# Performance work log

Measured on AMD Instinct MI355X. Metric: run time of the kernel, lower is better.

Reference implementation:

```python
import jax, jax.numpy as jnp
import numpy as np

B, S, D = 2, 2048, 1024
H = 16
HD = D // H  # 64


def setup_inputs() -> dict:
    key = jax.random.key(0)
    ks = jax.random.split(key, 9)
    scale = 1.0 / np.sqrt(D)
    x = jax.random.normal(ks[0], (B, S, D), dtype=jnp.float32)
    Wq = jax.random.normal(ks[1], (D, D), dtype=jnp.float32) * scale
    bq = jnp.zeros((D,), dtype=jnp.float32)
    Wk = jax.random.normal(ks[2], (D, D), dtype=jnp.float32) * scale
    bk = jnp.zeros((D,), dtype=jnp.float32)
    Wv = jax.random.normal(ks[3], (D, D), dtype=jnp.float32) * scale
    bv = jnp.zeros((D,), dtype=jnp.float32)
    Wo = jax.random.normal(ks[4], (D, D), dtype=jnp.float32) * scale
    bo = jnp.zeros((D,), dtype=jnp.float32)
    return {"x": x, "Wq": Wq, "bq": bq, "Wk": Wk, "bk": bk,
            "Wv": Wv, "bv": bv, "Wo": Wo, "bo": bo}


def reference(x, Wq, bq, Wk, bk, Wv, bv, Wo, bo):
    b, s, d = x.shape
    # QKV projections (PhotonicCore == dim->dim linear)
    Q = x @ Wq + bq
    K = x @ Wk + bk
    V = x @ Wv + bv
    # [B, H, S, HD]
    Q = Q.reshape(b, s, H, HD).transpose(0, 2, 1, 3)
    K = K.reshape(b, s, H, HD).transpose(0, 2, 1, 3)
    V = V.reshape(b, s, H, HD).transpose(0, 2, 1, 3)
    # full [B, H, S, S] scores, exactly as the original (unfused) module
    scores = jnp.einsum("bhqd,bhkd->bhqk", Q, K) / jnp.sqrt(jnp.asarray(HD, x.dtype))
    weights = jax.nn.softmax(scores, axis=-1)
    attn = jnp.einsum("bhqk,bhkd->bhqd", weights, V)
    attn = attn.transpose(0, 2, 1, 3).reshape(b, s, d)
    return attn @ Wo + bo
```

## Files before the change

### kernel.cpp

```cpp
#include <hip/hip_runtime.h>
#include <stdint.h>

typedef unsigned short u16;
typedef unsigned int u32;
typedef unsigned long long u64;
typedef __bf16 bf16x8 __attribute__((ext_vector_type(8)));
typedef float f32x4 __attribute__((ext_vector_type(4)));
typedef unsigned short u16x8 __attribute__((ext_vector_type(8)));
typedef unsigned short u16x4 __attribute__((ext_vector_type(4)));

#define QSCALE 0.1803368801111204f

static __device__ __forceinline__ u16 f2bf(float f) {
  unsigned u = __builtin_bit_cast(unsigned, f);
  u += 0x7fffu + ((u >> 16) & 1u);
  return (u16)(u >> 16);
}

static __device__ __forceinline__ bf16x8 ldfrag(const u16* p) {
  return *reinterpret_cast<const bf16x8*>(p);
}

static __device__ __forceinline__ void gll16(const u16* g, u16* l) {
  __builtin_amdgcn_global_load_lds(
      (const __attribute__((address_space(1))) void*)g,
      (__attribute__((address_space(3))) void*)l, 16, 0, 0);
}

static __device__ __forceinline__ u32 cvt_pk_bf16(float lo, float hi) {
  u32 r;
  asm("v_cvt_pk_bf16_f32 %0, %1, %2" : "=v"(r) : "v"(lo), "v"(hi));
  return r;
}

static __device__ __forceinline__ float fexp2(float x) {
  return __builtin_amdgcn_exp2f(x);
}

static __device__ __forceinline__ float fm3(float a, float b, float c) {
  return fmaxf(fmaxf(a, b), c);
}

__global__ __launch_bounds__(256) void cast_x_kernel(const float* __restrict__ x,
                                                     u16* __restrict__ xb) {
  int i = (blockIdx.x * 256 + threadIdx.x) * 8;
  const float4* p = reinterpret_cast<const float4*>(x + i);
  float4 a = p[0], b = p[1];
  u16x8 o;
  o[0] = f2bf(a.x); o[1] = f2bf(a.y); o[2] = f2bf(a.z); o[3] = f2bf(a.w);
  o[4] = f2bf(b.x); o[5] = f2bf(b.y); o[6] = f2bf(b.z); o[7] = f2bf(b.w);
  *reinterpret_cast<u16x8*>(xb + i) = o;
}

__global__ __launch_bounds__(256) void transpose_w_kernel(
    const float* __restrict__ Wq, const float* __restrict__ Wk,
    const float* __restrict__ Wv, const float* __restrict__ Wo,
    u16* __restrict__ WT) {
  __shared__ float tile[64][65];
  int z = blockIdx.z;
  const float* W = (z == 0) ? Wq : (z == 1) ? Wk : (z == 2) ? Wv : Wo;
  float wscale = (z == 0) ? QSCALE : 1.0f;
  u16* out = WT + (size_t)z * 1024 * 1024;
  int k0 = blockIdx.y * 64, n0 = blockIdx.x * 64;
  int t = threadIdx.x;
  int rr = t >> 4;
  int cc = (t & 15) * 4;
#pragma unroll
  for (int j = 0; j < 4; ++j) {
    int r = rr + 16 * j;
    float4 v = *reinterpret_cast<const float4*>(W + (size_t)(k0 + r) * 1024 + n0 + cc);
    tile[r][cc + 0] = v.x; tile[r][cc + 1] = v.y;
    tile[r][cc + 2] = v.z; tile[r][cc + 3] = v.w;
  }
  __syncthreads();
#pragma unroll
  for (int j = 0; j < 4; ++j) {
    int nl = rr + 16 * j;
    u16x4 o;
#pragma unroll
    for (int i2 = 0; i2 < 4; ++i2) o[i2] = f2bf(tile[cc + i2][nl] * wscale);
    *reinterpret_cast<u16x4*>(out + (size_t)(n0 + nl) * 1024 + k0 + cc) = o;
  }
}

template <int MODE>
static __device__ __forceinline__ void qkv_body(
    u16* smem, const u16* __restrict__ A, const u16* __restrict__ Wt,
    const float* __restrict__ bias, float bscale, u16* __restrict__ Out) {
  int t = threadIdx.x;
  int lane = t & 63, wave = t >> 6;
  int g = lane >> 4, c = lane & 15;
  int m0 = blockIdx.y * 128, n0 = blockIdx.x * 128;
  int wm = (wave >> 1) * 32, wn = (wave & 1) * 64;

  f32x4 acc[2][4] = {};

  const u16* Ag = A + (size_t)(m0 + (t >> 2)) * 1024 + (t & 3) * 8;
  const u16* Bg = Wt + (size_t)(n0 + (t >> 2)) * 1024 + (t & 3) * 8;

  u16* dstA = smem + t * 8;
  u16* dstB = smem + 4096 + t * 8;
  const int afo = (wm + c) * 32 + g * 8;
  const int bfo = 4096 + (wn + c) * 32 + g * 8;

  gll16(Ag, dstA);
  gll16(Bg, dstB);
  gll16(Ag + 32, dstA + 8192);
  gll16(Bg + 32, dstB + 8192);
  asm volatile("s_waitcnt vmcnt(2)" ::: "memory");
  __builtin_amdgcn_s_barrier();
  asm volatile("" ::: "memory");

  int cur = 0;
  for (int st = 0; st < 32; ++st) {
    if (st <= 29) {
      int nb = cur + 2; if (nb >= 3) nb -= 3;
      gll16(Ag + (st + 2) * 32, dstA + nb * 8192);
      gll16(Bg + (st + 2) * 32, dstB + nb * 8192);
    }
    const u16* buf = smem + cur * 8192;
    bf16x8 af[2], bfr[4];
#pragma unroll
    for (int i = 0; i < 2; ++i) af[i] = ldfrag(buf + afo + 16 * i * 32);
#pragma unroll
    for (int j = 0; j < 4; ++j) bfr[j] = ldfrag(buf + bfo + 16 * j * 32);
    __builtin_amdgcn_s_setprio(1);
#pragma unroll
    for (int i = 0; i < 2; ++i)
#pragma unroll
      for (int j = 0; j < 4; ++j) {
        if (MODE == 2)
          acc[i][j] = __builtin_amdgcn_mfma_f32_16x16x32_bf16(af[i], bfr[j], acc[i][j], 0, 0, 0);
        else
          acc[i][j] = __builtin_amdgcn_mfma_f32_16x16x32_bf16(bfr[j], af[i], acc[i][j], 0, 0, 0);
      }
    __builtin_amdgcn_s_setprio(0);

    if (st <= 29)
      asm volatile("s_waitcnt vmcnt(2)" ::: "memory");
    else if (st == 30)
      asm volatile("s_waitcnt vmcnt(0)" ::: "memory");
    if (st < 31) {
      __builtin_amdgcn_s_barrier();
      asm volatile("" ::: "memory");
    }
    ++cur; if (cur == 3) cur = 0;
  }

  if (MODE == 0) {
    int nj[4], hj[4], dj[4];
    f32x4 bbj[4];
#pragma unroll
    for (int j = 0; j < 4; ++j) {
      nj[j] = n0 + wn + 16 * j + 4 * g;
      hj[j] = nj[j] >> 6; dj[j] = nj[j] & 63;
      f32x4 bb = *reinterpret_cast<const f32x4*>(&bias[nj[j]]);
#pragma unroll
      for (int r = 0; r < 4; ++r) bbj[j][r] = bb[r] * bscale;
    }
#pragma unroll
    for (int i = 0; i < 2; ++i) {
      int m = m0 + wm + 16 * i + c;
      int b2 = m >> 11, s2 = m & 2047;
#pragma unroll
      for (int j = 0; j < 4; ++j) {
        u16x4 o4;
#pragma unroll
        for (int r = 0; r < 4; ++r) o4[r] = f2bf(acc[i][j][r] + bbj[j][r]);
        *reinterpret_cast<u16x4*>(
            Out + ((size_t)(b2 * 16 + hj[j]) * 2048 + s2) * 64 + dj[j]) = o4;
      }
    }
  } else {
    float bvj[4];
#pragma unroll
    for (int j = 0; j < 4; ++j) bvj[j] = bias[n0 + wn + 16 * j + c];
    u16* tb = smem;
    int b2 = m0 >> 11, s0 = m0 & 2047;
    int rdrow = t >> 3;
    int slot = t & 7;
    int sh_base = ((wave >> 1) & 1) * 32;
    __syncthreads();
#pragma unroll
    for (int half = 0; half < 2; ++half) {
      if ((wave >> 2) == half) {
#pragma unroll
        for (int i = 0; i < 2; ++i)
#pragma unroll
          for (int j = 0; j < 4; ++j) {
            u16x4 o4;
#pragma unroll
            for (int r = 0; r < 4; ++r) o4[r] = f2bf(acc[i][j][r] + bvj[j]);
            *reinterpret_cast<u16x4*>(
                &tb[(wn + 16 * j + c) * 72 + sh_base + 16 * i + 4 * g]) = o4;
          }
      }
      __syncthreads();
#pragma unroll
      for (int k = 0; k < 2; ++k) {
        int row = rdrow + 64 * k;
        u16x8 v = *reinterpret_cast<const u16x8*>(&tb[row * 72 + slot * 8]);
        int n = n0 + row, h2 = n >> 6, d2 = n & 63;
        *reinterpret_cast<u16x8*>(
            Out + ((size_t)(b2 * 16 + h2) * 64 + d2) * 2048 + s0 + half * 64 + slot * 8) = v;
      }
      if (half == 0) __syncthreads();
    }
  }
}

__global__ __launch_bounds__(512) void qkv_gemm_kernel(
    const u16* __restrict__ xb, const u16* __restrict__ WT,
    const float* __restrict__ bq, const float* __restrict__ bk,
    const float* __restrict__ bv,
    u16* __restrict__ Q, u16* __restrict__ K, u16* __restrict__ V) {
  __shared__ u16 smem[24576];
  int z = blockIdx.z;
  if (z == 0)      qkv_body<0>(smem, xb, WT, bq, QSCALE, Q);
  else if (z == 1) qkv_body<0>(smem, xb, WT + (size_t)1024 * 1024, bk, 1.0f, K);
  else             qkv_body<2>(smem, xb, WT + (size_t)2 * 1024 * 1024, bv, 1.0f, V);
}

__global__ __launch_bounds__(512) void oproj_kernel(
    const u16* __restrict__ A, const u16* __restrict__ Wt,
    const float* __restrict__ bias, float* __restrict__ out) {
  __shared__ u16 smem[24576];
  int t = threadIdx.x;
  int lane = t & 63, wave = t >> 6;
  int g = lane >> 4, c = lane & 15;
  int m0 = blockIdx.y * 128, n0 = blockIdx.x * 128;
  int wm = (wave >> 1) * 32, wn = (wave & 1) * 64;

  f32x4 acc[2][4] = {};

  const u16* Ag = A + (size_t)(m0 + (t >> 2)) * 1024 + (t & 3) * 8;
  const u16* Bg = Wt + (size_t)(n0 + (t >> 2)) * 1024 + (t & 3) * 8;
  u16* dstA = smem + t * 8;
  u16* dstB = smem + 4096 + t * 8;
  const int afo = (wm + c) * 32 + g * 8;
  const int bfo = 4096 + (wn + c) * 32 + g * 8;

  gll16(Ag, dstA);
  gll16(Bg, dstB);
  gll16(Ag + 32, dstA + 8192);
  gll16(Bg + 32, dstB + 8192);
  asm volatile("s_waitcnt vmcnt(2)" ::: "memory");
  __builtin_amdgcn_s_barrier();
  asm volatile("" ::: "memory");

  int cur = 0;
  for (int st = 0; st < 32; ++st) {
    if (st <= 29) {
      int nb = cur + 2; if (nb >= 3) nb -= 3;
      gll16(Ag + (st + 2) * 32, dstA + nb * 8192);
      gll16(Bg + (st + 2) * 32, dstB + nb * 8192);
    }
    const u16* buf = smem + cur * 8192;
    bf16x8 af[2], bfr[4];
#pragma unroll
    for (int i = 0; i < 2; ++i) af[i] = ldfrag(buf + afo + 16 * i * 32);
#pragma unroll
    for (int j = 0; j < 4; ++j) bfr[j] = ldfrag(buf + bfo + 16 * j * 32);
    __builtin_amdgcn_s_setprio(1);
#pragma unroll
    for (int i = 0; i < 2; ++i)
#pragma unroll
      for (int j = 0; j < 4; ++j)
        acc[i][j] = __builtin_amdgcn_mfma_f32_16x16x32_bf16(bfr[j], af[i], acc[i][j], 0, 0, 0);
    __builtin_amdgcn_s_setprio(0);

    if (st <= 29)
      asm volatile("s_waitcnt vmcnt(2)" ::: "memory");
    else if (st == 30)
      asm volatile("s_waitcnt vmcnt(0)" ::: "memory");
    if (st < 31) {
      __builtin_amdgcn_s_barrier();
      asm volatile("" ::: "memory");
    }
    ++cur; if (cur == 3) cur = 0;
  }

  f32x4 bbj[4];
#pragma unroll
  for (int j = 0; j < 4; ++j)
    bbj[j] = *reinterpret_cast<const f32x4*>(&bias[n0 + wn + 16 * j + 4 * g]);
#pragma unroll
  for (int i = 0; i < 2; ++i) {
    int m = m0 + wm + 16 * i + c;
#pragma unroll
    for (int j = 0; j < 4; ++j) {
      f32x4 v = acc[i][j] + bbj[j];
      *reinterpret_cast<f32x4*>(out + (size_t)m * 1024 + n0 + wn + 16 * j + 4 * g) = v;
    }
  }
}

__global__ __launch_bounds__(512) void attn_kernel(
    const u16* __restrict__ Q, const u16* __restrict__ K,
    const u16* __restrict__ V, u16* __restrict__ attn) {
  __shared__ u16 Kf[3][4096];
  __shared__ u16 Vt[3][4096];
  __shared__ u16 Pf[8][512];

  const int t = threadIdx.x;
  const int lane = t & 63, w = t >> 6;
  const int g = lane >> 4, c = lane & 15;

  int flat = blockIdx.x + 16 * (blockIdx.y + 16 * blockIdx.z);
  int sw = (flat & 7) * 64 + (flat >> 3);
  const int b = sw >> 8, h = (sw >> 4) & 15, q0 = (sw & 15) * 128;

  const u16* Qh = Q + ((size_t)(b * 16 + h) * 2048) * 64;
  const u16* Kh = K + ((size_t)(b * 16 + h) * 2048) * 64;
  const u16* VTh = V + ((size_t)(b * 16 + h) * 64) * 2048;

  const int qw = q0 + w * 16;
  bf16x8 qf0 = ldfrag(Qh + (size_t)(qw + c) * 64 + 8 * g);
  bf16x8 qf1 = ldfrag(Qh + (size_t)(qw + c) * 64 + 32 + 8 * g);

  bf16x8 ones;
  {
    u16x8 tmp;
#pragma unroll
    for (int l = 0; l < 8; ++l) tmp[l] = 0x3F80;
    ones = __builtin_bit_cast(bf16x8, tmp);
  }

  const u16* ksrc = Kh + (size_t)(16 * ((w >> 1) & 3) + c) * 64 + 32 * (w & 1) + 8 * g;
  const u16* vsrc = VTh + (size_t)(8 * w + (lane >> 3)) * 2048 +
                    (((lane & 7) ^ ((lane >> 3) & 7)) * 8);

  const int koff = g * 128 + c * 8;
  int vb_off[2];
#pragma unroll
  for (int m = 0; m < 2; ++m)
    vb_off[m] = c * 64 + (((4 * m + g) ^ (c & 7)) * 8);
  const int pa_off = (g * 16 + c) * 8;

  f32x4 o[4] = {};
  f32x4 lsum = {};
  float mrow = -3e38f;

  gll16(ksrc, &Kf[0][t * 8]);
  gll16(vsrc, &Vt[0][t * 8]);
  gll16(ksrc + 4096, &Kf[1][t * 8]);
  gll16(vsrc + 64, &Vt[1][t * 8]);
  asm volatile("s_waitcnt vmcnt(2)" ::: "memory");
  __builtin_amdgcn_s_barrier();
  asm volatile("" ::: "memory");

  int cur = 0;
  for (int tt32 = 0; tt32 < 32; ++tt32) {
    if (tt32 <= 29) {
      int nb = cur + 2; if (nb >= 3) nb -= 3;
      gll16(ksrc + (size_t)(tt32 + 2) * 4096, &Kf[nb][t * 8]);
      gll16(vsrc + (size_t)(tt32 + 2) * 64, &Vt[nb][t * 8]);
    }

    const u16* kb = &Kf[cur][koff];
    f32x4 st[4];
    __builtin_amdgcn_s_setprio(1);
#pragma unroll
    for (int t4 = 0; t4 < 4; ++t4) {
      f32x4 acc = {};
      acc = __builtin_amdgcn_mfma_f32_16x16x32_bf16(
          ldfrag(kb + t4 * 1024), qf0, acc, 0, 0, 0);
      st[t4] = __builtin_amdgcn_mfma_f32_16x16x32_bf16(
          ldfrag(kb + t4 * 1024 + 512), qf1, acc, 0, 0, 0);
    }
    __builtin_amdgcn_s_setprio(0);

    float u1 = fm3(fm3(st[0][0], st[0][1], st[0][2]),
                   fm3(st[0][3], st[1][0], st[1][1]),
                   fm3(st[1][2], st[1][3], st[2][0]));
    float u2 = fm3(fm3(st[2][1], st[2][2], st[2][3]),
                   fm3(st[3][0], st[3][1], st[3][2]), st[3][3]);
    float tm = fmaxf(u1, u2);
    tm = fmaxf(tm, __shfl_xor(tm, 16));
    tm = fmaxf(tm, __shfl_xor(tm, 32));
    const bool grow = __any(tm > mrow + 8.0f);
    if (grow) {
      float nm = fmaxf(mrow, tm);
      float f = fexp2(mrow - nm);
      mrow = nm;
#pragma unroll
      for (int r = 0; r < 4; ++r) {
        float fr = __shfl(f, 4 * g + r);
        lsum[r] *= fr;
#pragma unroll
        for (int j = 0; j < 4; ++j) o[j][r] *= fr;
      }
    }
#pragma unroll
    for (int t4 = 0; t4 < 4; ++t4)
#pragma unroll
      for (int r = 0; r < 4; ++r) st[t4][r] = fexp2(st[t4][r] - mrow);

    u32* pd = (u32*)&Pf[w][0];
#pragma unroll
    for (int m = 0; m < 2; ++m) {
#pragma unroll
      for (int tp = 0; tp < 2; ++tp) {
        int t4 = 2 * m + tp;
        u32 w0 = cvt_pk_bf16(st[t4][0], st[t4][1]);
        u32 w1 = cvt_pk_bf16(st[t4][2], st[t4][3]);
        int gp = (2 * t4 + (g >> 1)) & 3;
        int base = (gp * 16 + c) * 4 + 2 * (g & 1);
        *reinterpret_cast<u64*>(&pd[base]) = (u64)w0 | ((u64)w1 << 32);
      }
      bf16x8 pa = ldfrag(&Pf[w][pa_off]);
      __builtin_amdgcn_s_setprio(1);
#pragma unroll
      for (int j = 0; j < 4; ++j) {
        bf16x8 vb = ldfrag(&Vt[cur][vb_off[m] + j * 1024]);
        o[j] = __builtin_amdgcn_mfma_f32_16x16x32_bf16(pa, vb, o[j], 0, 0, 0);
      }
      lsum = __builtin_amdgcn_mfma_f32_16x16x32_bf16(pa, ones, lsum, 0, 0, 0);
      __builtin_amdgcn_s_setprio(0);
    }

    if (tt32 <= 29)
      asm volatile("s_waitcnt vmcnt(2)" ::: "memory");
    else if (tt32 == 30)
      asm volatile("s_waitcnt vmcnt(0)" ::: "memory");
    if (tt32 < 31) {
      __builtin_amdgcn_s_barrier();
      asm volatile("" ::: "memory");
    }
    ++cur; if (cur == 3) cur = 0;
  }

  float rinv[4];
#pragma unroll
  for (int r = 0; r < 4; ++r) rinv[r] = 1.f / lsum[r];
#pragma unroll
  for (int j = 0; j < 4; ++j)
#pragma unroll
    for (int r = 0; r < 4; ++r) {
      int s = qw + 4 * g + r;
      attn[(size_t)(b * 2048 + s) * 1024 + h * 64 + 16 * j + c] = f2bf(o[j][r] * rinv[r]);
    }
}

extern "C" void kernel_launch(void* const* d_in, const int* in_sizes, int n_in,
                              void* d_out, int out_size, void* d_ws, size_t ws_size,
                              hipStream_t stream) {
  const float* x  = (const float*)d_in[0];
  const float* Wq = (const float*)d_in[1];
  const float* bq = (const float*)d_in[2];
  const float* Wk = (const float*)d_in[3];
  const float* bk = (const float*)d_in[4];
  const float* Wv = (const float*)d_in[5];
  const float* bv = (const float*)d_in[6];
  const float* Wo = (const float*)d_in[7];
  const float* bo = (const float*)d_in[8];
  float* out = (float*)d_out;
  u16* ws = (u16*)d_ws;

  u16* xb    = ws;
  u16* WT    = ws + (size_t)4 * 1024 * 1024;
  u16* Qb    = ws + (size_t)8 * 1024 * 1024;
  u16* Kb    = ws + (size_t)12 * 1024 * 1024;
  u16* Vb    = ws + (size_t)16 * 1024 * 1024;
  u16* attnb = xb;

  cast_x_kernel<<<2048, 256, 0, stream>>>(x, xb);
  transpose_w_kernel<<<dim3(16, 16, 4), 256, 0, stream>>>(Wq, Wk, Wv, Wo, WT);
  qkv_gemm_kernel<<<dim3(8, 32, 3), 512, 0, stream>>>(xb, WT, bq, bk, bv, Qb, Kb, Vb);
  attn_kernel<<<dim3(16, 16, 2), 512, 0, stream>>>(Qb, Kb, Vb, attnb);
  oproj_kernel<<<dim3(8, 32), 512, 0, stream>>>(attnb, WT + (size_t)3 * 1024 * 1024, bo, out);
}
```

Baseline: 124.3 us.

## Process two query subtiles per wave in attention and merge prep kernels

The attention kernel now runs 4 waves of 256 threads, each handling 32 query rows as two 16-row subtiles. Each K fragment and V fragment read from LDS is reused across both subtiles, which halves LDS traffic per MFMA and doubles the loads each thread issues to stage K/V tiles. The x cast and weight transpose kernels are merged into a single launch to save one kernel launch. Register pressure goes up, and fewer waves are left per block to hide latency.

```diff
diff --git a/kernel.cpp b/kernel.cpp
--- a/kernel.cpp
+++ b/kernel.cpp
@@ -41,28 +41,30 @@
   return fmaxf(fmaxf(a, b), c);
 }
 
-__global__ __launch_bounds__(256) void cast_x_kernel(const float* __restrict__ x,
-                                                     u16* __restrict__ xb) {
-  int i = (blockIdx.x * 256 + threadIdx.x) * 8;
-  const float4* p = reinterpret_cast<const float4*>(x + i);
-  float4 a = p[0], b = p[1];
-  u16x8 o;
-  o[0] = f2bf(a.x); o[1] = f2bf(a.y); o[2] = f2bf(a.z); o[3] = f2bf(a.w);
-  o[4] = f2bf(b.x); o[5] = f2bf(b.y); o[6] = f2bf(b.z); o[7] = f2bf(b.w);
-  *reinterpret_cast<u16x8*>(xb + i) = o;
-}
-
-__global__ __launch_bounds__(256) void transpose_w_kernel(
+__global__ __launch_bounds__(256) void prep_kernel(
+    const float* __restrict__ x,
     const float* __restrict__ Wq, const float* __restrict__ Wk,
     const float* __restrict__ Wv, const float* __restrict__ Wo,
-    u16* __restrict__ WT) {
+    u16* __restrict__ xb, u16* __restrict__ WT) {
   __shared__ float tile[64][65];
-  int z = blockIdx.z;
+  int bid = blockIdx.x;
+  int t = threadIdx.x;
+  if (bid < 2048) {
+    int i = (bid * 256 + t) * 8;
+    const float4* p = reinterpret_cast<const float4*>(x + i);
+    float4 a = p[0], b = p[1];
+    u16x8 o;
+    o[0] = f2bf(a.x); o[1] = f2bf(a.y); o[2] = f2bf(a.z); o[3] = f2bf(a.w);
+    o[4] = f2bf(b.x); o[5] = f2bf(b.y); o[6] = f2bf(b.z); o[7] = f2bf(b.w);
+    *reinterpret_cast<u16x8*>(xb + i) = o;
+    return;
+  }
+  int r0 = bid - 2048;
+  int z = r0 >> 8, rem = r0 & 255;
+  int n0 = (rem & 15) * 64, k0 = (rem >> 4) * 64;
   const float* W = (z == 0) ? Wq : (z == 1) ? Wk : (z == 2) ? Wv : Wo;
   float wscale = (z == 0) ? QSCALE : 1.0f;
   u16* out = WT + (size_t)z * 1024 * 1024;
-  int k0 = blockIdx.y * 64, n0 = blockIdx.x * 64;
-  int t = threadIdx.x;
   int rr = t >> 4;
   int cc = (t & 15) * 4;
 #pragma unroll
@@ -295,12 +297,12 @@
   }
 }
 
-__global__ __launch_bounds__(512) void attn_kernel(
+__global__ __launch_bounds__(256) void attn_kernel(
     const u16* __restrict__ Q, const u16* __restrict__ K,
     const u16* __restrict__ V, u16* __restrict__ attn) {
   __shared__ u16 Kf[3][4096];
   __shared__ u16 Vt[3][4096];
-  __shared__ u16 Pf[8][512];
+  __shared__ u16 Pf[4][1024];
 
   const int t = threadIdx.x;
   const int lane = t & 63, w = t >> 6;
@@ -314,9 +316,13 @@
   const u16* Kh = K + ((size_t)(b * 16 + h) * 2048) * 64;
   const u16* VTh = V + ((size_t)(b * 16 + h) * 64) * 2048;
 
-  const int qw = q0 + w * 16;
-  bf16x8 qf0 = ldfrag(Qh + (size_t)(qw + c) * 64 + 8 * g);
-  bf16x8 qf1 = ldfrag(Qh + (size_t)(qw + c) * 64 + 32 + 8 * g);
+  const int qw = q0 + w * 32;
+  bf16x8 qf[2][2];
+#pragma unroll
+  for (int qs = 0; qs < 2; ++qs) {
+    qf[qs][0] = ldfrag(Qh + (size_t)(qw + 16 * qs + c) * 64 + 8 * g);
+    qf[qs][1] = ldfrag(Qh + (size_t)(qw + 16 * qs + c) * 64 + 32 + 8 * g);
+  }
 
   bf16x8 ones;
   {
@@ -326,9 +332,23 @@
     ones = __builtin_bit_cast(bf16x8, tmp);
   }
 
-  const u16* ksrc = Kh + (size_t)(16 * ((w >> 1) & 3) + c) * 64 + 32 * (w & 1) + 8 * g;
-  const u16* vsrc = VTh + (size_t)(8 * w + (lane >> 3)) * 2048 +
-                    (((lane & 7) ^ ((lane >> 3) & 7)) * 8);
+  const u16* ksrc[2];
+  u16* kdst[2];
+#pragma unroll
+  for (int i = 0; i < 2; ++i) {
+    int unit = ((w * 2 + i) << 6) | lane;
+    int cc = unit & 15, gg = (unit >> 4) & 3, uu = (unit >> 6) & 1, t4 = (unit >> 7) & 3;
+    ksrc[i] = Kh + (size_t)(16 * t4 + cc) * 64 + 32 * uu + 8 * gg;
+    kdst[i] = (u16*)&Kf[0][0] + unit * 8;
+  }
+  const u16* vsrc[2];
+  u16* vdst[2];
+#pragma unroll
+  for (int i = 0; i < 2; ++i) {
+    int d = 16 * w + 8 * i + (lane >> 3);
+    vsrc[i] = VTh + (size_t)d * 2048 + (((lane & 7) ^ ((lane >> 3) & 7)) * 8);
+    vdst[i] = (u16*)&Vt[0][0] + (16 * w + 8 * i) * 64 + lane * 8;
+  }
 
   const int koff = g * 128 + c * 8;
   int vb_off[2];
@@ -337,109 +357,129 @@
     vb_off[m] = c * 64 + (((4 * m + g) ^ (c & 7)) * 8);
   const int pa_off = (g * 16 + c) * 8;
 
-  f32x4 o[4] = {};
-  f32x4 lsum = {};
-  float mrow = -3e38f;
-
-  gll16(ksrc, &Kf[0][t * 8]);
-  gll16(vsrc, &Vt[0][t * 8]);
-  gll16(ksrc + 4096, &Kf[1][t * 8]);
-  gll16(vsrc + 64, &Vt[1][t * 8]);
-  asm volatile("s_waitcnt vmcnt(2)" ::: "memory");
+  f32x4 o[2][4] = {};
+  f32x4 lsum[2] = {};
+  float mrow[2] = {-3e38f, -3e38f};
+
+#pragma unroll
+  for (int i = 0; i < 2; ++i) { gll16(ksrc[i], kdst[i]); gll16(vsrc[i], vdst[i]); }
+#pragma unroll
+  for (int i = 0; i < 2; ++i) {
+    gll16(ksrc[i] + 4096, kdst[i] + 4096);
+    gll16(vsrc[i] + 64, vdst[i] + 4096);
+  }
+  asm volatile("s_waitcnt vmcnt(4)" ::: "memory");
   __builtin_amdgcn_s_barrier();
   asm volatile("" ::: "memory");
 
   int cur = 0;
-  for (int tt32 = 0; tt32 < 32; ++tt32) {
-    if (tt32 <= 29) {
+  for (int tt = 0; tt < 32; ++tt) {
+    if (tt <= 29) {
       int nb = cur + 2; if (nb >= 3) nb -= 3;
-      gll16(ksrc + (size_t)(tt32 + 2) * 4096, &Kf[nb][t * 8]);
-      gll16(vsrc + (size_t)(tt32 + 2) * 64, &Vt[nb][t * 8]);
+#pragma unroll
+      for (int i = 0; i < 2; ++i) {
+        gll16(ksrc[i] + (size_t)(tt + 2) * 4096, kdst[i] + nb * 4096);
+        gll16(vsrc[i] + (size_t)(tt + 2) * 64, vdst[i] + nb * 4096);
+      }
     }
 
     const u16* kb = &Kf[cur][koff];
-    f32x4 st[4];
+    f32x4 st[4][2];
     __builtin_amdgcn_s_setprio(1);
 #pragma unroll
     for (int t4 = 0; t4 < 4; ++t4) {
-      f32x4 acc = {};
-      acc = __builtin_amdgcn_mfma_f32_16x16x32_bf16(
-          ldfrag(kb + t4 * 1024), qf0, acc, 0, 0, 0);
-      st[t4] = __builtin_amdgcn_mfma_f32_16x16x32_bf16(
-          ldfrag(kb + t4 * 1024 + 512), qf1, acc, 0, 0, 0);
+      bf16x8 k0 = ldfrag(kb + t4 * 1024);
+      bf16x8 k1 = ldfrag(kb + t4 * 1024 + 512);
+#pragma unroll
+      for (int qs = 0; qs < 2; ++qs) {
+        f32x4 acc = {};
+        acc = __builtin_amdgcn_mfma_f32_16x16x32_bf16(k0, qf[qs][0], acc, 0, 0, 0);
+        st[t4][qs] = __builtin_amdgcn_mfma_f32_16x16x32_bf16(k1, qf[qs][1], acc, 0, 0, 0);
+      }
     }
     __builtin_amdgcn_s_setprio(0);
 
-    float u1 = fm3(fm3(st[0][0], st[0][1], st[0][2]),
-                   fm3(st[0][3], st[1][0], st[1][1]),
-                   fm3(st[1][2], st[1][3], st[2][0]));
-    float u2 = fm3(fm3(st[2][1], st[2][2], st[2][3]),
-                   fm3(st[3][0], st[3][1], st[3][2]), st[3][3]);
-    float tm = fmaxf(u1, u2);
-    tm = fmaxf(tm, __shfl_xor(tm, 16));
-    tm = fmaxf(tm, __shfl_xor(tm, 32));
-    const bool grow = __any(tm > mrow + 8.0f);
-    if (grow) {
-      float nm = fmaxf(mrow, tm);
-      float f = fexp2(mrow - nm);
-      mrow = nm;
-#pragma unroll
-      for (int r = 0; r < 4; ++r) {
-        float fr = __shfl(f, 4 * g + r);
-        lsum[r] *= fr;
-#pragma unroll
-        for (int j = 0; j < 4; ++j) o[j][r] *= fr;
-      }
-    }
-#pragma unroll
-    for (int t4 = 0; t4 < 4; ++t4)
-#pragma unroll
-      for (int r = 0; r < 4; ++r) st[t4][r] = fexp2(st[t4][r] - mrow);
-
-    u32* pd = (u32*)&Pf[w][0];
+#pragma unroll
+    for (int qs = 0; qs < 2; ++qs) {
+      float u1 = fm3(fm3(st[0][qs][0], st[0][qs][1], st[0][qs][2]),
+                     fm3(st[0][qs][3], st[1][qs][0], st[1][qs][1]),
+                     fm3(st[1][qs][2], st[1][qs][3], st[2][qs][0]));
+      float u2 = fm3(fm3(st[2][qs][1], st[2][qs][2], st[2][qs][3]),
+                     fm3(st[3][qs][0], st[3][qs][1], st[3][qs][2]), st[3][qs][3]);
+      float tm = fmaxf(u1, u2);
+      tm = fmaxf(tm, __shfl_xor(tm, 16));
+      tm = fmaxf(tm, __shfl_xor(tm, 32));
+      const bool grow = __any(tm > mrow[qs] + 8.0f);
+      if (grow) {
+        float nm = fmaxf(mrow[qs], tm);
+        float f = fexp2(mrow[qs] - nm);
+        mrow[qs] = nm;
+#pragma unroll
+        for (int r = 0; r < 4; ++r) {
+          float fr = __shfl(f, 4 * g + r);
+          lsum[qs][r] *= fr;
+#pragma unroll
+          for (int j = 0; j < 4; ++j) o[qs][j][r] *= fr;
+        }
+      }
+#pragma unroll
+      for (int t4 = 0; t4 < 4; ++t4)
+#pragma unroll
+        for (int r = 0; r < 4; ++r) st[t4][qs][r] = fexp2(st[t4][qs][r] - mrow[qs]);
+    }
+
 #pragma unroll
     for (int m = 0; m < 2; ++m) {
-#pragma unroll
-      for (int tp = 0; tp < 2; ++tp) {
-        int t4 = 2 * m + tp;
-        u32 w0 = cvt_pk_bf16(st[t4][0], st[t4][1]);
-        u32 w1 = cvt_pk_bf16(st[t4][2], st[t4][3]);
-        int gp = (2 * t4 + (g >> 1)) & 3;
-        int base = (gp * 16 + c) * 4 + 2 * (g & 1);
-        *reinterpret_cast<u64*>(&pd[base]) = (u64)w0 | ((u64)w1 << 32);
-      }
-      bf16x8 pa = ldfrag(&Pf[w][pa_off]);
-      __builtin_amdgcn_s_setprio(1);
-#pragma unroll
-      for (int j = 0; j < 4; ++j) {
-        bf16x8 vb = ldfrag(&Vt[cur][vb_off[m] + j * 1024]);
-        o[j] = __builtin_amdgcn_mfma_f32_16x16x32_bf16(pa, vb, o[j], 0, 0, 0);
-      }
-      lsum = __builtin_amdgcn_mfma_f32_16x16x32_bf16(pa, ones, lsum, 0, 0, 0);
-      __builtin_amdgcn_s_setprio(0);
-    }
-
-    if (tt32 <= 29)
-      asm volatile("s_waitcnt vmcnt(2)" ::: "memory");
-    else if (tt32 == 30)
+      bf16x8 vb[4];
+#pragma unroll
+      for (int j = 0; j < 4; ++j) vb[j] = ldfrag(&Vt[cur][vb_off[m] + j * 1024]);
+#pragma unroll
+      for (int qs = 0; qs < 2; ++qs) {
+        u32* pd = (u32*)&Pf[w][qs * 512];
+#pragma unroll
+        for (int tp = 0; tp < 2; ++tp) {
+          int t4 = 2 * m + tp;
+          u32 w0 = cvt_pk_bf16(st[t4][qs][0], st[t4][qs][1]);
+          u32 w1 = cvt_pk_bf16(st[t4][qs][2], st[t4][qs][3]);
+          int gp = (2 * t4 + (g >> 1)) & 3;
+          int base = (gp * 16 + c) * 4 + 2 * (g & 1);
+          *reinterpret_cast<u64*>(&pd[base]) = (u64)w0 | ((u64)w1 << 32);
+        }
+        bf16x8 pa = ldfrag(&Pf[w][qs * 512 + pa_off]);
+        __builtin_amdgcn_s_setprio(1);
+#pragma unroll
+        for (int j = 0; j < 4; ++j)
+          o[qs][j] = __builtin_amdgcn_mfma_f32_16x16x32_bf16(pa, vb[j], o[qs][j], 0, 0, 0);
+        lsum[qs] = __builtin_amdgcn_mfma_f32_16x16x32_bf16(pa, ones, lsum[qs], 0, 0, 0);
+        __builtin_amdgcn_s_setprio(0);
+      }
+    }
+
+    if (tt <= 29)
+      asm volatile("s_waitcnt vmcnt(4)" ::: "memory");
+    else if (tt == 30)
       asm volatile("s_waitcnt vmcnt(0)" ::: "memory");
-    if (tt32 < 31) {
+    if (tt < 31) {
       __builtin_amdgcn_s_barrier();
       asm volatile("" ::: "memory");
     }
     ++cur; if (cur == 3) cur = 0;
   }
 
-  float rinv[4];
-#pragma unroll
-  for (int r = 0; r < 4; ++r) rinv[r] = 1.f / lsum[r];
-#pragma unroll
-  for (int j = 0; j < 4; ++j)
-#pragma unroll
-    for (int r = 0; r < 4; ++r) {
-      int s = qw + 4 * g + r;
-      attn[(size_t)(b * 2048 + s) * 1024 + h * 64 + 16 * j + c] = f2bf(o[j][r] * rinv[r]);
-    }
+#pragma unroll
+  for (int qs = 0; qs < 2; ++qs) {
+    float rinv[4];
+#pragma unroll
+    for (int r = 0; r < 4; ++r) rinv[r] = 1.f / lsum[qs][r];
+#pragma unroll
+    for (int j = 0; j < 4; ++j)
+#pragma unroll
+      for (int r = 0; r < 4; ++r) {
+        int s = qw + 16 * qs + 4 * g + r;
+        attn[(size_t)(b * 2048 + s) * 1024 + h * 64 + 16 * j + c] =
+            f2bf(o[qs][j][r] * rinv[r]);
+      }
+  }
 }
 
 extern "C" void kernel_launch(void* const* d_in, const int* in_sizes, int n_in,
@@ -464,9 +504,8 @@
   u16* Vb    = ws + (size_t)16 * 1024 * 1024;
   u16* attnb = xb;
 
-  cast_x_kernel<<<2048, 256, 0, stream>>>(x, xb);
-  transpose_w_kernel<<<dim3(16, 16, 4), 256, 0, stream>>>(Wq, Wk, Wv, Wo, WT);
+  prep_kernel<<<3072, 256, 0, stream>>>(x, Wq, Wk, Wv, Wo, xb, WT);
   qkv_gemm_kernel<<<dim3(8, 32, 3), 512, 0, stream>>>(xb, WT, bq, bk, bv, Qb, Kb, Vb);
-  attn_kernel<<<dim3(16, 16, 2), 512, 0, stream>>>(Qb, Kb, Vb, attnb);
+  attn_kernel<<<dim3(16, 16, 2), 256, 0, stream>>>(Qb, Kb, Vb, attnb);
   oproj_kernel<<<dim3(8, 32), 512, 0, stream>>>(attnb, WT + (size_t)3 * 1024 * 1024, bo, out);
 }
```

Measured after the change: 136.1 us. 9.6% more time.
